# Performance work log

Hardware: AMD Instinct MI355X
Metric: run time of the kernel (lower is better)

## Reference

```python
import jax, jax.numpy as jnp
import numpy as np

DIM = 1024
HEADS = 16
DIM_HEAD = 64
INNER = HEADS * DIM_HEAD  # 1024
RANK = 16
ALPHA = 8.0
LORA_SCALE = ALPHA / RANK  # 0.5
NUM_PATCHES = 256
NUM_FRAMES = 8
T = NUM_PATCHES * NUM_FRAMES  # 2048
B = 2
MEM = 16
EPS = 1e-5


def _block_causal_mask(num_patches, num_frames):
    # generate_mask_matrix: causal across frames, full within a frame
    tril = np.tril(np.ones((num_frames, num_frames), dtype=np.int32))
    m = np.kron(tril, np.ones((num_patches, num_patches), dtype=np.int32))
    return jnp.asarray(m[None, None])  # [1,1,T,T]


def setup_inputs() -> dict:
    key = jax.random.key(0)
    ks = jax.random.split(key, 16)
    s_in = 1.0 / np.sqrt(DIM)
    s_r = 1.0 / np.sqrt(RANK)
    return {
        "x": jax.random.normal(ks[0], (B, T, DIM), jnp.float32),
        "memory_tokens": jax.random.normal(ks[1], (B, MEM, DIM), jnp.float32),
        "ln_g": jnp.ones((DIM,), jnp.float32),
        "ln_b": jnp.zeros((DIM,), jnp.float32),
        "w_qkv": jax.random.normal(ks[2], (DIM, 3 * INNER), jnp.float32) * s_in,
        "qA": jax.random.normal(ks[3], (DIM, RANK), jnp.float32) * s_in,
        "qB": jax.random.normal(ks[4], (RANK, INNER), jnp.float32) * s_r * 0.02,
        "kA": jax.random.normal(ks[5], (DIM, RANK), jnp.float32) * s_in,
        "kB": jax.random.normal(ks[6], (RANK, INNER), jnp.float32) * s_r * 0.02,
        "vA": jax.random.normal(ks[7], (DIM, RANK), jnp.float32) * s_in,
        "vB": jax.random.normal(ks[8], (RANK, INNER), jnp.float32) * s_r * 0.02,
        "w_out": jax.random.normal(ks[9], (INNER, DIM), jnp.float32) / np.sqrt(INNER),
        "b_out": jnp.zeros((DIM,), jnp.float32),
        "outA": jax.random.normal(ks[10], (INNER, RANK), jnp.float32) / np.sqrt(INNER),
        "outB": jax.random.normal(ks[11], (RANK, DIM), jnp.float32) * s_r * 0.02,
        "bias_mask": _block_causal_mask(NUM_PATCHES, NUM_FRAMES),
    }


def _lora(x, A, Bm):
    return LORA_SCALE * ((x @ A) @ Bm)


def reference(x, memory_tokens, ln_g, ln_b, w_qkv, qA, qB, kA, kB, vA, vB,
              w_out, b_out, outA, outB, bias_mask):
    # LayerNorm
    mu = jnp.mean(x, axis=-1, keepdims=True)
    var = jnp.var(x, axis=-1, keepdims=True)
    xn = (x - mu) * jax.lax.rsqrt(var + EPS) * ln_g + ln_b

    qkv = xn @ w_qkv  # [B,T,3*INNER]
    q, k, v = jnp.split(qkv, 3, axis=-1)
    # LoRA deltas (memory_tokens enables the LoRA path)
    q = q + _lora(xn, qA, qB)
    k = k + _lora(xn, kA, kB)
    v = v + _lora(xn, vA, vB)

    def to_heads(t):
        b, n, _ = t.shape
        return t.reshape(b, n, HEADS, DIM_HEAD).transpose(0, 2, 1, 3)  # b h n d

    q, k, v = to_heads(q), to_heads(k), to_heads(v)
    scale = DIM_HEAD ** -0.5
    dots = jnp.einsum('bhid,bhjd->bhij', q, k) * scale  # [B,H,T,T]
    dots = jnp.where(bias_mask[:, :, :q.shape[2], :q.shape[2]] == 0, -jnp.inf, dots)
    attn = jax.nn.softmax(dots, axis=-1)  # dropout p=0.0
    out = jnp.einsum('bhij,bhjd->bhid', attn, v)
    out = out.transpose(0, 2, 1, 3).reshape(x.shape[0], x.shape[1], INNER)
    out = out @ w_out + b_out
    out = out + _lora(out, outA, outB)  # lora_on_out
    return out
```

## Files before the change

### kernel.cpp

```cpp
#include <hip/hip_runtime.h>


#define DIMSZ 1024
#define TSEQ  2048
#define MTOK  4096

typedef __attribute__((ext_vector_type(8))) short bf16x8;
typedef __attribute__((ext_vector_type(4))) short bf16x4;
typedef __attribute__((ext_vector_type(4))) float f32x4;

__device__ __forceinline__ unsigned short f2bf(float f) {
  unsigned int u = __float_as_uint(f);
  u += 0x7fffu + ((u >> 16) & 1u);
  return (unsigned short)(u >> 16);
}
__device__ __forceinline__ float bf2f(unsigned short s) {
  return __uint_as_float(((unsigned int)s) << 16);
}
__device__ __forceinline__ unsigned int cvtpk_bf16(float a, float b) {
  unsigned int d;
  asm("v_cvt_pk_bf16_f32 %0, %1, %2" : "=v"(d) : "v"(a), "v"(b));
  return d;
}
__device__ __forceinline__ void gload16(const void* g, void* l) {
  __builtin_amdgcn_global_load_lds((const __attribute__((address_space(1))) void*)g,
                                   (__attribute__((address_space(3))) void*)l, 16, 0, 0);
}

__global__ __launch_bounds__(256) void ln_kernel(const float* __restrict__ x,
    const float* __restrict__ g, const float* __restrict__ b,
    unsigned short* __restrict__ xn) {
  int row = blockIdx.x;
  int tid = threadIdx.x;
  const float4* xr = (const float4*)(x + (size_t)row * DIMSZ);
  float4 v = xr[tid];
  float s  = v.x + v.y + v.z + v.w;
  float s2 = v.x*v.x + v.y*v.y + v.z*v.z + v.w*v.w;
  #pragma unroll
  for (int off = 32; off > 0; off >>= 1) {
    s  += __shfl_xor(s, off, 64);
    s2 += __shfl_xor(s2, off, 64);
  }
  __shared__ float red[8];
  int wid = tid >> 6, lane = tid & 63;
  if (lane == 0) { red[wid] = s; red[wid + 4] = s2; }
  __syncthreads();
  s  = red[0] + red[1] + red[2] + red[3];
  s2 = red[4] + red[5] + red[6] + red[7];
  float mu  = s * (1.0f / DIMSZ);
  float var = s2 * (1.0f / DIMSZ) - mu * mu;
  float rstd = rsqrtf(var + 1e-5f);
  float4 gg = ((const float4*)g)[tid];
  float4 bb = ((const float4*)b)[tid];
  ushort4 o;
  o.x = f2bf((v.x - mu) * rstd * gg.x + bb.x);
  o.y = f2bf((v.y - mu) * rstd * gg.y + bb.y);
  o.z = f2bf((v.z - mu) * rstd * gg.z + bb.z);
  o.w = f2bf((v.w - mu) * rstd * gg.w + bb.w);
  ((ushort4*)(xn + (size_t)row * DIMSZ))[tid] = o;
}

__global__ __launch_bounds__(64) void woutA_kernel(const float* __restrict__ w_out,
    const float* __restrict__ outA, float* __restrict__ WA) {
  int k = blockIdx.x;
  int l = threadIdx.x;
  float a[16];
  #pragma unroll
  for (int r = 0; r < 16; ++r) a[r] = 0.f;
  for (int c = l; c < DIMSZ; c += 64) {
    float w = w_out[(size_t)k * DIMSZ + c];
    const float* ap = outA + (size_t)c * 16;
    #pragma unroll
    for (int r = 0; r < 16; ++r) a[r] += w * ap[r];
  }
  #pragma unroll
  for (int r = 0; r < 16; ++r) {
    #pragma unroll
    for (int off = 32; off > 0; off >>= 1) a[r] += __shfl_xor(a[r], off, 64);
  }
  if (l < 16) WA[k * 16 + l] = a[l];
}

__global__ __launch_bounds__(256) void beff_kernel(const float* __restrict__ b_out,
    const float* __restrict__ outA, const float* __restrict__ outB,
    float* __restrict__ beff) {
  int tid = threadIdx.x, wid = tid >> 6, lane = tid & 63;
  float a[16];
  #pragma unroll
  for (int r = 0; r < 16; ++r) a[r] = 0.f;
  for (int c = tid; c < DIMSZ; c += 256) {
    float bo = b_out[c];
    const float* ap = outA + (size_t)c * 16;
    #pragma unroll
    for (int r = 0; r < 16; ++r) a[r] += bo * ap[r];
  }
  #pragma unroll
  for (int r = 0; r < 16; ++r) {
    #pragma unroll
    for (int off = 32; off > 0; off >>= 1) a[r] += __shfl_xor(a[r], off, 64);
  }
  __shared__ float sh[4][16];
  if (lane == 0) {
    #pragma unroll
    for (int r = 0; r < 16; ++r) sh[wid][r] = a[r];
  }
  __syncthreads();
  __shared__ float tt[16];
  if (tid < 16) tt[tid] = sh[0][tid] + sh[1][tid] + sh[2][tid] + sh[3][tid];
  __syncthreads();
  for (int n = tid; n < DIMSZ; n += 256) {
    float l = 0.f;
    #pragma unroll
    for (int r = 0; r < 16; ++r) l += tt[r] * outB[(size_t)r * DIMSZ + n];
    beff[n] = b_out[n] + 0.5f * l;
  }
}

__global__ __launch_bounds__(256) void foldT4_kernel(
    const float* __restrict__ w_qkv, const float* __restrict__ w_out,
    const float* __restrict__ qA, const float* __restrict__ qB,
    const float* __restrict__ kA, const float* __restrict__ kB,
    const float* __restrict__ vA, const float* __restrict__ vB,
    const float* __restrict__ WA, const float* __restrict__ outB,
    unsigned short* __restrict__ WqkvT, unsigned short* __restrict__ WoutT) {
  __shared__ float Bs[16][64];
  __shared__ unsigned short Ts[64][72];
  int z = blockIdx.z;
  const float *W, *A, *Bf;
  unsigned short* Wt;
  int ldw, col_off;
  if (z == 0)      { W = w_qkv; ldw = 3072; col_off = 0;    A = qA; Bf = qB;   Wt = WqkvT; }
  else if (z == 1) { W = w_qkv; ldw = 3072; col_off = 1024; A = kA; Bf = kB;   Wt = WqkvT + 1048576; }
  else if (z == 2) { W = w_qkv; ldw = 3072; col_off = 2048; A = vA; Bf = vB;   Wt = WqkvT + 2097152; }
  else             { W = w_out; ldw = 1024; col_off = 0;    A = WA; Bf = outB; Wt = WoutT; }
  int n0 = blockIdx.x * 64, k0 = blockIdx.y * 64;
  int tx = threadIdx.x, ty = threadIdx.y;
  for (int r = ty; r < 16; r += 4) Bs[r][tx] = Bf[(size_t)r * DIMSZ + n0 + tx];
  __syncthreads();
  for (int k = ty; k < 64; k += 4) {
    int kk = k0 + k;
    float w = W[(size_t)kk * ldw + col_off + n0 + tx];
    const float* Ar = A + (size_t)kk * 16;
    float lora = 0.f;
    #pragma unroll
    for (int r = 0; r < 16; ++r) lora += Ar[r] * Bs[r][tx];
    Ts[tx][k] = f2bf(w + 0.5f * lora);
  }
  __syncthreads();
  for (int n = ty; n < 64; n += 4)
    Wt[(size_t)(n0 + n) * DIMSZ + k0 + tx] = Ts[n][tx];
}

template<int MODE>
__global__ __launch_bounds__(256) void gemm_kernel(
    const unsigned short* __restrict__ Abf, const unsigned short* __restrict__ Bt,
    int K,
    unsigned short* __restrict__ Qo, unsigned short* __restrict__ Ko,
    unsigned short* __restrict__ Vto,
    const float* __restrict__ bias, float* __restrict__ Cout) {
  __shared__ __align__(16) char As[128 * 64 * 2];
  __shared__ __align__(16) char Bs[128 * 64 * 2];
  int n0 = blockIdx.x * 128;
  int m0 = blockIdx.y * 128;
  int tid = threadIdx.x;
  int wid = tid >> 6, lane = tid & 63;
  int wr = wid >> 1, wc = wid & 1;
  int hi = lane >> 4;
  f32x4 acc[4][4];
  #pragma unroll
  for (int i = 0; i < 4; ++i)
    #pragma unroll
    for (int j = 0; j < 4; ++j) acc[i][j] = (f32x4){0.f, 0.f, 0.f, 0.f};

  const char* gA = (const char*)Abf;
  const char* gB = (const char*)Bt;
  int Kb2 = K * 2;
  int nkt = K >> 6;
  for (int kt = 0; kt < nkt; ++kt) {
    #pragma unroll
    for (int j = 0; j < 4; ++j) {
      int it = wid * 4 + j;
      int p = it * 1024 + lane * 16;
      int row = p >> 7, colb = p & 127;
      int L = colb ^ ((row & 7) << 4);
      gload16(gA + (size_t)(m0 + row) * Kb2 + kt * 128 + L, As + it * 1024);
      gload16(gB + (size_t)(n0 + row) * Kb2 + kt * 128 + L, Bs + it * 1024);
    }
    __syncthreads();
    #pragma unroll
    for (int ks = 0; ks < 2; ++ks) {
      int kb = ks * 64 + hi * 16;
      bf16x8 af[4], bfr[4];
      #pragma unroll
      for (int m = 0; m < 4; ++m) {
        int row = wr * 64 + m * 16 + (lane & 15);
        af[m] = *(const bf16x8*)(As + row * 128 + (kb ^ ((row & 7) << 4)));
      }
      #pragma unroll
      for (int n = 0; n < 4; ++n) {
        int row = wc * 64 + n * 16 + (lane & 15);
        bfr[n] = *(const bf16x8*)(Bs + row * 128 + (kb ^ ((row & 7) << 4)));
      }
      __builtin_amdgcn_s_setprio(1);
      #pragma unroll
      for (int n = 0; n < 4; ++n)
        #pragma unroll
        for (int m = 0; m < 4; ++m)
          acc[n][m] = __builtin_amdgcn_mfma_f32_16x16x32_bf16(bfr[n], af[m], acc[n][m], 0, 0, 0);
      __builtin_amdgcn_s_setprio(0);
    }
    __syncthreads();
  }

  if (MODE == 0) {
    int sec  = n0 >> 10;
    int nloc = (n0 & 1023) + wc * 64;
    int h = nloc >> 6;
    int mbase = m0 + wr * 64;
    #pragma unroll
    for (int m = 0; m < 4; ++m) {
      int gm = mbase + m * 16 + (lane & 15);
      int bb = gm >> 11, t = gm & 2047;
      #pragma unroll
      for (int n = 0; n < 4; ++n) {
        int dloc = n * 16 + hi * 4;
        if (sec == 2) {
          #pragma unroll
          for (int r = 0; r < 4; ++r)
            Vto[((size_t)((bb * 16 + h) * 64 + dloc + r)) * TSEQ + t] = f2bf(acc[n][m][r]);
        } else {
          bf16x4 o;
          #pragma unroll
          for (int r = 0; r < 4; ++r) o[r] = (short)f2bf(acc[n][m][r]);
          size_t idx = ((size_t)(bb * 16 + h) * TSEQ + t) * 64 + dloc;
          *(bf16x4*)((sec == 0 ? Qo : Ko) + idx) = o;
        }
      }
    }
  } else {
    int mbase = m0 + wr * 64;
    int nbase = n0 + wc * 64;
    #pragma unroll
    for (int m = 0; m < 4; ++m) {
      int t = mbase + m * 16 + (lane & 15);
      #pragma unroll
      for (int n = 0; n < 4; ++n) {
        int c = nbase + n * 16 + hi * 4;
        float4 bs = *(const float4*)(bias + c);
        float4 o;
        o.x = acc[n][m][0] + bs.x;
        o.y = acc[n][m][1] + bs.y;
        o.z = acc[n][m][2] + bs.z;
        o.w = acc[n][m][3] + bs.w;
        *(float4*)(Cout + (size_t)t * DIMSZ + c) = o;
      }
    }
  }
}

__global__ __launch_bounds__(256, 4) void attn_kernel(
    const unsigned short* __restrict__ Qg, const unsigned short* __restrict__ Kg,
    const unsigned short* __restrict__ Vt, unsigned short* __restrict__ Orow) {
  __shared__ __align__(16) char KsB[2][64 * 128];
  __shared__ __align__(16) char VsB[2][64 * 128];
  __shared__ __align__(16) char Ps[4][16 * 128];
  int bh = blockIdx.x;
  int y  = blockIdx.y;
  int qt = (y < 16) ? (31 - y) : (y - 16);
  int b = bh >> 4, h = bh & 15;
  int tid = threadIdx.x, wid = tid >> 6, lane = tid & 63;
  int hi = lane >> 4, lo = lane & 15;
  const char* Qb = (const char*)(Qg + (size_t)bh * TSEQ * 64);
  const char* Kb = (const char*)(Kg + (size_t)bh * TSEQ * 64);
  const char* Vb = (const char*)(Vt + (size_t)bh * 64 * TSEQ);
  int q0 = qt * 64;

  int srow = tid >> 3;
  int scol = ((tid & 7) << 4) ^ ((srow & 7) << 4);

  const float qscale = 0.18033688f;
  bf16x8 qf[2];
  {
    int row = q0 + wid * 16 + lo;
    #pragma unroll
    for (int ks = 0; ks < 2; ++ks) {
      bf16x8 raw = *(const bf16x8*)(Qb + (size_t)row * 128 + ks * 64 + hi * 16);
      bf16x8 sc;
      #pragma unroll
      for (int i = 0; i < 8; ++i)
        sc[i] = (short)f2bf(bf2f((unsigned short)raw[i]) * qscale);
      qf[ks] = sc;
    }
  }

  f32x4 Oacc[4];
  #pragma unroll
  for (int df = 0; df < 4; ++df) Oacc[df] = (f32x4){0.f, 0.f, 0.f, 0.f};
  float mrun = -INFINITY, lrun = 0.f;

  char* Pw = Ps[wid];
  char* pbase = Pw + lo * 128;
  int pswz = (lo & 7) << 4;

  int nkt = ((qt >> 2) + 1) << 2;

  {
    const char* ksrc = Kb + (size_t)srow * 128 + scol;
    gload16(ksrc,               KsB[0] + tid * 16);
    gload16(ksrc + 32 * 128,    KsB[0] + tid * 16 + 4096);
    const char* vsrc = Vb + (size_t)srow * (TSEQ * 2) + scol;
    gload16(vsrc,               VsB[0] + tid * 16);
    gload16(vsrc + 32 * (TSEQ * 2), VsB[0] + tid * 16 + 4096);
  }

  for (int kt = 0; kt < nkt; ++kt) {
    __syncthreads();
    if (kt + 1 < nkt) {
      int k0n = (kt + 1) << 6;
      char* kd = KsB[(kt + 1) & 1];
      const char* ksrc = Kb + (size_t)(k0n + srow) * 128 + scol;
      gload16(ksrc,            kd + tid * 16);
      gload16(ksrc + 32 * 128, kd + tid * 16 + 4096);
    }
    if (kt) {
      char* vd = VsB[kt & 1];
      const char* vsrc = Vb + (size_t)srow * (TSEQ * 2) + (kt << 7) + scol;
      gload16(vsrc,                   vd + tid * 16);
      gload16(vsrc + 32 * (TSEQ * 2), vd + tid * 16 + 4096);
    }
    const char* Kbuf = KsB[kt & 1];

    f32x4 s[4];
    #pragma unroll
    for (int nf = 0; nf < 4; ++nf) s[nf] = (f32x4){0.f, 0.f, 0.f, 0.f};
    #pragma unroll
    for (int ks = 0; ks < 2; ++ks) {
      int kb = ks * 64 + hi * 16;
      bf16x8 kf[4];
      #pragma unroll
      for (int nf = 0; nf < 4; ++nf) {
        int row = nf * 16 + lo;
        kf[nf] = *(const bf16x8*)(Kbuf + row * 128 + (kb ^ ((row & 7) << 4)));
      }
      __builtin_amdgcn_s_setprio(1);
      #pragma unroll
      for (int nf = 0; nf < 4; ++nf)
        s[nf] = __builtin_amdgcn_mfma_f32_16x16x32_bf16(kf[nf], qf[ks], s[nf], 0, 0, 0);
      __builtin_amdgcn_s_setprio(0);
    }

    if (kt) {
      const char* Vbuf = VsB[(kt - 1) & 1];
      #pragma unroll
      for (int ks2 = 0; ks2 < 2; ++ks2) {
        int kb = ks2 * 64 + hi * 16;
        bf16x8 pf = *(const bf16x8*)(Pw + lo * 128 + (kb ^ pswz));
        bf16x8 vf[4];
        #pragma unroll
        for (int df = 0; df < 4; ++df) {
          int row = df * 16 + lo;
          vf[df] = *(const bf16x8*)(Vbuf + row * 128 + (kb ^ ((row & 7) << 4)));
        }
        __builtin_amdgcn_s_setprio(1);
        #pragma unroll
        for (int df = 0; df < 4; ++df)
          Oacc[df] = __builtin_amdgcn_mfma_f32_16x16x32_bf16(vf[df], pf, Oacc[df], 0, 0, 0);
        __builtin_amdgcn_s_setprio(0);
      }
    }

    float a0 = fmaxf(fmaxf(s[0][0], s[0][1]), fmaxf(s[0][2], s[0][3]));
    float a1 = fmaxf(fmaxf(s[1][0], s[1][1]), fmaxf(s[1][2], s[1][3]));
    float a2 = fmaxf(fmaxf(s[2][0], s[2][1]), fmaxf(s[2][2], s[2][3]));
    float a3 = fmaxf(fmaxf(s[3][0], s[3][1]), fmaxf(s[3][2], s[3][3]));
    float mx = fmaxf(fmaxf(a0, a1), fmaxf(a2, a3));
    mx = fmaxf(mx, __shfl_xor(mx, 16, 64));
    mx = fmaxf(mx, __shfl_xor(mx, 32, 64));

    if (!__all(mx <= mrun + 8.0f)) {
      float mn = fmaxf(mrun, mx);
      float al = exp2f(mrun - mn);
      mrun = mn;
      lrun *= al;
      #pragma unroll
      for (int df = 0; df < 4; ++df)
        #pragma unroll
        for (int r = 0; r < 4; ++r) Oacc[df][r] *= al;
    }

    float rs0 = 0.f, rs1 = 0.f, rs2 = 0.f, rs3 = 0.f;
    #pragma unroll
    for (int nf = 0; nf < 4; ++nf) {
      float p0 = exp2f(s[nf][0] - mrun);
      float p1 = exp2f(s[nf][1] - mrun);
      float p2 = exp2f(s[nf][2] - mrun);
      float p3 = exp2f(s[nf][3] - mrun);
      s[nf][0] = p0; s[nf][1] = p1; s[nf][2] = p2; s[nf][3] = p3;
      rs0 += p0; rs1 += p1; rs2 += p2; rs3 += p3;
    }
    lrun += (rs0 + rs1) + (rs2 + rs3);

    #pragma unroll
    for (int nf = 0; nf < 4; ++nf) {
      unsigned int w0 = cvtpk_bf16(s[nf][0], s[nf][1]);
      unsigned int w1 = cvtpk_bf16(s[nf][2], s[nf][3]);
      uint2 pr; pr.x = w0; pr.y = w1;
      *(uint2*)(pbase + ((nf * 32 + hi * 8) ^ pswz)) = pr;
    }
  }

  __syncthreads();
  {
    const char* Vbuf = VsB[(nkt - 1) & 1];
    #pragma unroll
    for (int ks2 = 0; ks2 < 2; ++ks2) {
      int kb = ks2 * 64 + hi * 16;
      bf16x8 pf = *(const bf16x8*)(Pw + lo * 128 + (kb ^ pswz));
      bf16x8 vf[4];
      #pragma unroll
      for (int df = 0; df < 4; ++df) {
        int row = df * 16 + lo;
        vf[df] = *(const bf16x8*)(Vbuf + row * 128 + (kb ^ ((row & 7) << 4)));
      }
      __builtin_amdgcn_s_setprio(1);
      #pragma unroll
      for (int df = 0; df < 4; ++df)
        Oacc[df] = __builtin_amdgcn_mfma_f32_16x16x32_bf16(vf[df], pf, Oacc[df], 0, 0, 0);
      __builtin_amdgcn_s_setprio(0);
    }
  }

  lrun += __shfl_xor(lrun, 16, 64);
  lrun += __shfl_xor(lrun, 32, 64);
  float inv = 1.0f / lrun;
  int t = q0 + wid * 16 + lo;
  size_t rowbase = ((size_t)(b * TSEQ + t)) * DIMSZ + h * 64;
  #pragma unroll
  for (int df = 0; df < 4; ++df) {
    bf16x4 o;
    #pragma unroll
    for (int r = 0; r < 4; ++r) o[r] = (short)f2bf(Oacc[df][r] * inv);
    *(bf16x4*)(Orow + rowbase + df * 16 + hi * 4) = o;
  }
}

extern "C" void kernel_launch(void* const* d_in, const int* in_sizes, int n_in,
                              void* d_out, int out_size, void* d_ws, size_t ws_size,
                              hipStream_t stream) {
  (void)in_sizes; (void)n_in; (void)out_size; (void)ws_size;
  const float* x     = (const float*)d_in[0];
  const float* ln_g  = (const float*)d_in[2];
  const float* ln_b  = (const float*)d_in[3];
  const float* w_qkv = (const float*)d_in[4];
  const float* qA    = (const float*)d_in[5];
  const float* qB    = (const float*)d_in[6];
  const float* kA    = (const float*)d_in[7];
  const float* kB    = (const float*)d_in[8];
  const float* vA    = (const float*)d_in[9];
  const float* vB    = (const float*)d_in[10];
  const float* w_out = (const float*)d_in[11];
  const float* b_out = (const float*)d_in[12];
  const float* outA  = (const float*)d_in[13];
  const float* outB  = (const float*)d_in[14];

  char* ws = (char*)d_ws;
  unsigned short* xn    = (unsigned short*)(ws);
  unsigned short* WqkvT = (unsigned short*)(ws + 8388608);
  unsigned short* WoutT = (unsigned short*)(ws + 14680064);
  float*          WA    = (float*)(ws + 16777216);
  float*          beff  = (float*)(ws + 16842752);
  unsigned short* Qb    = (unsigned short*)(ws + 16846848);
  unsigned short* Kb    = (unsigned short*)(ws + 25235456);
  unsigned short* Vtb   = (unsigned short*)(ws + 33624064);
  unsigned short* Orow  = xn;
  float* outp = (float*)d_out;

  ln_kernel<<<MTOK, 256, 0, stream>>>(x, ln_g, ln_b, xn);
  woutA_kernel<<<DIMSZ, 64, 0, stream>>>(w_out, outA, WA);
  beff_kernel<<<1, 256, 0, stream>>>(b_out, outA, outB, beff);
  dim3 fb(64, 4);
  foldT4_kernel<<<dim3(16, 16, 4), fb, 0, stream>>>(w_qkv, w_out, qA, qB, kA, kB,
                                                    vA, vB, WA, outB, WqkvT, WoutT);

  gemm_kernel<0><<<dim3(24, 32), 256, 0, stream>>>(xn, WqkvT, DIMSZ, Qb, Kb, Vtb, nullptr, nullptr);
  attn_kernel<<<dim3(32, 32), 256, 0, stream>>>(Qb, Kb, Vtb, Orow);
  gemm_kernel<1><<<dim3(8, 32), 256, 0, stream>>>(Orow, WoutT, DIMSZ, nullptr, nullptr, nullptr, beff, outp);
}
```

Measured before the change: 142.9 us.

## Double attention query tile per wave and merge prep kernels into one launch

The attention kernel now gives each wave 32 query rows (two 16-row MFMA fragments) instead of 16. Each K/V tile loaded into LDS is therefore reused across twice as many queries, and the grid is halved. Separately, layernorm, the w_out·outA fold and the effective-bias computation are merged into one launch to cut launch overhead. In exchange, register pressure roughly doubles (launch bounds drop to 2 blocks per SM). Coarser 128-row tiles also waste more work on the block-causal boundary and leave fewer blocks to balance the load.

```diff
diff --git a/kernel.cpp b/kernel.cpp
--- a/kernel.cpp
+++ b/kernel.cpp
@@ -27,92 +27,88 @@
                                    (__attribute__((address_space(3))) void*)l, 16, 0, 0);
 }
 
-__global__ __launch_bounds__(256) void ln_kernel(const float* __restrict__ x,
-    const float* __restrict__ g, const float* __restrict__ b,
-    unsigned short* __restrict__ xn) {
-  int row = blockIdx.x;
-  int tid = threadIdx.x;
-  const float4* xr = (const float4*)(x + (size_t)row * DIMSZ);
-  float4 v = xr[tid];
-  float s  = v.x + v.y + v.z + v.w;
-  float s2 = v.x*v.x + v.y*v.y + v.z*v.z + v.w*v.w;
-  #pragma unroll
-  for (int off = 32; off > 0; off >>= 1) {
-    s  += __shfl_xor(s, off, 64);
-    s2 += __shfl_xor(s2, off, 64);
-  }
+__global__ __launch_bounds__(256) void prep_kernel(const float* __restrict__ x,
+    const float* __restrict__ g, const float* __restrict__ bln,
+    const float* __restrict__ w_out, const float* __restrict__ outA,
+    const float* __restrict__ b_out, const float* __restrict__ outB,
+    unsigned short* __restrict__ xn, float* __restrict__ WA,
+    float* __restrict__ beff) {
   __shared__ float red[8];
-  int wid = tid >> 6, lane = tid & 63;
-  if (lane == 0) { red[wid] = s; red[wid + 4] = s2; }
-  __syncthreads();
-  s  = red[0] + red[1] + red[2] + red[3];
-  s2 = red[4] + red[5] + red[6] + red[7];
-  float mu  = s * (1.0f / DIMSZ);
-  float var = s2 * (1.0f / DIMSZ) - mu * mu;
-  float rstd = rsqrtf(var + 1e-5f);
-  float4 gg = ((const float4*)g)[tid];
-  float4 bb = ((const float4*)b)[tid];
-  ushort4 o;
-  o.x = f2bf((v.x - mu) * rstd * gg.x + bb.x);
-  o.y = f2bf((v.y - mu) * rstd * gg.y + bb.y);
-  o.z = f2bf((v.z - mu) * rstd * gg.z + bb.z);
-  o.w = f2bf((v.w - mu) * rstd * gg.w + bb.w);
-  ((ushort4*)(xn + (size_t)row * DIMSZ))[tid] = o;
-}
-
-__global__ __launch_bounds__(64) void woutA_kernel(const float* __restrict__ w_out,
-    const float* __restrict__ outA, float* __restrict__ WA) {
-  int k = blockIdx.x;
-  int l = threadIdx.x;
-  float a[16];
-  #pragma unroll
-  for (int r = 0; r < 16; ++r) a[r] = 0.f;
-  for (int c = l; c < DIMSZ; c += 64) {
-    float w = w_out[(size_t)k * DIMSZ + c];
-    const float* ap = outA + (size_t)c * 16;
-    #pragma unroll
-    for (int r = 0; r < 16; ++r) a[r] += w * ap[r];
-  }
-  #pragma unroll
-  for (int r = 0; r < 16; ++r) {
-    #pragma unroll
-    for (int off = 32; off > 0; off >>= 1) a[r] += __shfl_xor(a[r], off, 64);
-  }
-  if (l < 16) WA[k * 16 + l] = a[l];
-}
-
-__global__ __launch_bounds__(256) void beff_kernel(const float* __restrict__ b_out,
-    const float* __restrict__ outA, const float* __restrict__ outB,
-    float* __restrict__ beff) {
+  __shared__ float sh[4][16];
+  __shared__ float tt[16];
+  int bid = blockIdx.x;
   int tid = threadIdx.x, wid = tid >> 6, lane = tid & 63;
-  float a[16];
-  #pragma unroll
-  for (int r = 0; r < 16; ++r) a[r] = 0.f;
-  for (int c = tid; c < DIMSZ; c += 256) {
-    float bo = b_out[c];
-    const float* ap = outA + (size_t)c * 16;
-    #pragma unroll
-    for (int r = 0; r < 16; ++r) a[r] += bo * ap[r];
-  }
-  #pragma unroll
-  for (int r = 0; r < 16; ++r) {
-    #pragma unroll
-    for (int off = 32; off > 0; off >>= 1) a[r] += __shfl_xor(a[r], off, 64);
-  }
-  __shared__ float sh[4][16];
-  if (lane == 0) {
-    #pragma unroll
-    for (int r = 0; r < 16; ++r) sh[wid][r] = a[r];
-  }
-  __syncthreads();
-  __shared__ float tt[16];
-  if (tid < 16) tt[tid] = sh[0][tid] + sh[1][tid] + sh[2][tid] + sh[3][tid];
-  __syncthreads();
-  for (int n = tid; n < DIMSZ; n += 256) {
-    float l = 0.f;
-    #pragma unroll
-    for (int r = 0; r < 16; ++r) l += tt[r] * outB[(size_t)r * DIMSZ + n];
-    beff[n] = b_out[n] + 0.5f * l;
+  if (bid < MTOK) {
+    int row = bid;
+    const float4* xr = (const float4*)(x + (size_t)row * DIMSZ);
+    float4 v = xr[tid];
+    float s  = v.x + v.y + v.z + v.w;
+    float s2 = v.x*v.x + v.y*v.y + v.z*v.z + v.w*v.w;
+    #pragma unroll
+    for (int off = 32; off > 0; off >>= 1) {
+      s  += __shfl_xor(s, off, 64);
+      s2 += __shfl_xor(s2, off, 64);
+    }
+    if (lane == 0) { red[wid] = s; red[wid + 4] = s2; }
+    __syncthreads();
+    s  = red[0] + red[1] + red[2] + red[3];
+    s2 = red[4] + red[5] + red[6] + red[7];
+    float mu  = s * (1.0f / DIMSZ);
+    float var = s2 * (1.0f / DIMSZ) - mu * mu;
+    float rstd = rsqrtf(var + 1e-5f);
+    float4 gg = ((const float4*)g)[tid];
+    float4 bb = ((const float4*)bln)[tid];
+    ushort4 o;
+    o.x = f2bf((v.x - mu) * rstd * gg.x + bb.x);
+    o.y = f2bf((v.y - mu) * rstd * gg.y + bb.y);
+    o.z = f2bf((v.z - mu) * rstd * gg.z + bb.z);
+    o.w = f2bf((v.w - mu) * rstd * gg.w + bb.w);
+    ((ushort4*)(xn + (size_t)row * DIMSZ))[tid] = o;
+  } else if (bid < MTOK + 256) {
+    int k = (bid - MTOK) * 4 + wid;
+    float a[16];
+    #pragma unroll
+    for (int r = 0; r < 16; ++r) a[r] = 0.f;
+    for (int c = lane; c < DIMSZ; c += 64) {
+      float w = w_out[(size_t)k * DIMSZ + c];
+      const float* ap = outA + (size_t)c * 16;
+      #pragma unroll
+      for (int r = 0; r < 16; ++r) a[r] += w * ap[r];
+    }
+    #pragma unroll
+    for (int r = 0; r < 16; ++r) {
+      #pragma unroll
+      for (int off = 32; off > 0; off >>= 1) a[r] += __shfl_xor(a[r], off, 64);
+    }
+    if (lane < 16) WA[k * 16 + lane] = a[lane];
+  } else {
+    float a[16];
+    #pragma unroll
+    for (int r = 0; r < 16; ++r) a[r] = 0.f;
+    for (int c = tid; c < DIMSZ; c += 256) {
+      float bo = b_out[c];
+      const float* ap = outA + (size_t)c * 16;
+      #pragma unroll
+      for (int r = 0; r < 16; ++r) a[r] += bo * ap[r];
+    }
+    #pragma unroll
+    for (int r = 0; r < 16; ++r) {
+      #pragma unroll
+      for (int off = 32; off > 0; off >>= 1) a[r] += __shfl_xor(a[r], off, 64);
+    }
+    if (lane == 0) {
+      #pragma unroll
+      for (int r = 0; r < 16; ++r) sh[wid][r] = a[r];
+    }
+    __syncthreads();
+    if (tid < 16) tt[tid] = sh[0][tid] + sh[1][tid] + sh[2][tid] + sh[3][tid];
+    __syncthreads();
+    for (int n = tid; n < DIMSZ; n += 256) {
+      float l = 0.f;
+      #pragma unroll
+      for (int r = 0; r < 16; ++r) l += tt[r] * outB[(size_t)r * DIMSZ + n];
+      beff[n] = b_out[n] + 0.5f * l;
+    }
   }
 }
 
@@ -258,30 +254,31 @@
   }
 }
 
-__global__ __launch_bounds__(256, 4) void attn_kernel(
+__global__ __launch_bounds__(256, 2) void attn_kernel(
     const unsigned short* __restrict__ Qg, const unsigned short* __restrict__ Kg,
     const unsigned short* __restrict__ Vt, unsigned short* __restrict__ Orow) {
   __shared__ __align__(16) char KsB[2][64 * 128];
   __shared__ __align__(16) char VsB[2][64 * 128];
-  __shared__ __align__(16) char Ps[4][16 * 128];
+  __shared__ __align__(16) char Ps[4][32 * 128];
   int bh = blockIdx.x;
   int y  = blockIdx.y;
-  int qt = (y < 16) ? (31 - y) : (y - 16);
+  int qt = (y < 8) ? (15 - y) : (y - 8);
   int b = bh >> 4, h = bh & 15;
   int tid = threadIdx.x, wid = tid >> 6, lane = tid & 63;
   int hi = lane >> 4, lo = lane & 15;
   const char* Qb = (const char*)(Qg + (size_t)bh * TSEQ * 64);
   const char* Kb = (const char*)(Kg + (size_t)bh * TSEQ * 64);
   const char* Vb = (const char*)(Vt + (size_t)bh * 64 * TSEQ);
-  int q0 = qt * 64;
+  int q0 = qt * 128;
 
   int srow = tid >> 3;
   int scol = ((tid & 7) << 4) ^ ((srow & 7) << 4);
 
   const float qscale = 0.18033688f;
-  bf16x8 qf[2];
-  {
-    int row = q0 + wid * 16 + lo;
+  bf16x8 qf[2][2];
+  #pragma unroll
+  for (int m = 0; m < 2; ++m) {
+    int row = q0 + wid * 32 + m * 16 + lo;
     #pragma unroll
     for (int ks = 0; ks < 2; ++ks) {
       bf16x8 raw = *(const bf16x8*)(Qb + (size_t)row * 128 + ks * 64 + hi * 16);
@@ -289,20 +286,22 @@
       #pragma unroll
       for (int i = 0; i < 8; ++i)
         sc[i] = (short)f2bf(bf2f((unsigned short)raw[i]) * qscale);
-      qf[ks] = sc;
-    }
-  }
-
-  f32x4 Oacc[4];
+      qf[m][ks] = sc;
+    }
+  }
+
+  f32x4 Oacc[2][4];
   #pragma unroll
-  for (int df = 0; df < 4; ++df) Oacc[df] = (f32x4){0.f, 0.f, 0.f, 0.f};
-  float mrun = -INFINITY, lrun = 0.f;
+  for (int m = 0; m < 2; ++m)
+    #pragma unroll
+    for (int df = 0; df < 4; ++df) Oacc[m][df] = (f32x4){0.f, 0.f, 0.f, 0.f};
+  float mrun[2] = {-INFINITY, -INFINITY};
+  float lrun[2] = {0.f, 0.f};
 
   char* Pw = Ps[wid];
-  char* pbase = Pw + lo * 128;
   int pswz = (lo & 7) << 4;
 
-  int nkt = ((qt >> 2) + 1) << 2;
+  int nkt = ((qt >> 1) + 1) << 2;
 
   {
     const char* ksrc = Kb + (size_t)srow * 128 + scol;
@@ -330,9 +329,11 @@
     }
     const char* Kbuf = KsB[kt & 1];
 
-    f32x4 s[4];
-    #pragma unroll
-    for (int nf = 0; nf < 4; ++nf) s[nf] = (f32x4){0.f, 0.f, 0.f, 0.f};
+    f32x4 s[2][4];
+    #pragma unroll
+    for (int m = 0; m < 2; ++m)
+      #pragma unroll
+      for (int nf = 0; nf < 4; ++nf) s[m][nf] = (f32x4){0.f, 0.f, 0.f, 0.f};
     #pragma unroll
     for (int ks = 0; ks < 2; ++ks) {
       int kb = ks * 64 + hi * 16;
@@ -344,8 +345,10 @@
       }
       __builtin_amdgcn_s_setprio(1);
       #pragma unroll
-      for (int nf = 0; nf < 4; ++nf)
-        s[nf] = __builtin_amdgcn_mfma_f32_16x16x32_bf16(kf[nf], qf[ks], s[nf], 0, 0, 0);
+      for (int m = 0; m < 2; ++m)
+        #pragma unroll
+        for (int nf = 0; nf < 4; ++nf)
+          s[m][nf] = __builtin_amdgcn_mfma_f32_16x16x32_bf16(kf[nf], qf[m][ks], s[m][nf], 0, 0, 0);
       __builtin_amdgcn_s_setprio(0);
     }
 
@@ -354,8 +357,10 @@
       #pragma unroll
       for (int ks2 = 0; ks2 < 2; ++ks2) {
         int kb = ks2 * 64 + hi * 16;
-        bf16x8 pf = *(const bf16x8*)(Pw + lo * 128 + (kb ^ pswz));
-        bf16x8 vf[4];
+        bf16x8 pf[2], vf[4];
+        #pragma unroll
+        for (int m = 0; m < 2; ++m)
+          pf[m] = *(const bf16x8*)(Pw + (m * 16 + lo) * 128 + (kb ^ pswz));
         #pragma unroll
         for (int df = 0; df < 4; ++df) {
           int row = df * 16 + lo;
@@ -363,49 +368,61 @@
         }
         __builtin_amdgcn_s_setprio(1);
         #pragma unroll
+        for (int m = 0; m < 2; ++m)
+          #pragma unroll
+          for (int df = 0; df < 4; ++df)
+            Oacc[m][df] = __builtin_amdgcn_mfma_f32_16x16x32_bf16(vf[df], pf[m], Oacc[m][df], 0, 0, 0);
+        __builtin_amdgcn_s_setprio(0);
+      }
+    }
+
+    float mx[2];
+    #pragma unroll
+    for (int m = 0; m < 2; ++m) {
+      float a0 = fmaxf(fmaxf(s[m][0][0], s[m][0][1]), fmaxf(s[m][0][2], s[m][0][3]));
+      float a1 = fmaxf(fmaxf(s[m][1][0], s[m][1][1]), fmaxf(s[m][1][2], s[m][1][3]));
+      float a2 = fmaxf(fmaxf(s[m][2][0], s[m][2][1]), fmaxf(s[m][2][2], s[m][2][3]));
+      float a3 = fmaxf(fmaxf(s[m][3][0], s[m][3][1]), fmaxf(s[m][3][2], s[m][3][3]));
+      float v = fmaxf(fmaxf(a0, a1), fmaxf(a2, a3));
+      v = fmaxf(v, __shfl_xor(v, 16, 64));
+      v = fmaxf(v, __shfl_xor(v, 32, 64));
+      mx[m] = v;
+    }
+    int ok = (mx[0] <= mrun[0] + 8.0f) & (mx[1] <= mrun[1] + 8.0f);
+    if (!__all(ok)) {
+      #pragma unroll
+      for (int m = 0; m < 2; ++m) {
+        float mn = fmaxf(mrun[m], mx[m]);
+        float al = exp2f(mrun[m] - mn);
+        mrun[m] = mn;
+        lrun[m] *= al;
+        #pragma unroll
         for (int df = 0; df < 4; ++df)
-          Oacc[df] = __builtin_amdgcn_mfma_f32_16x16x32_bf16(vf[df], pf, Oacc[df], 0, 0, 0);
-        __builtin_amdgcn_s_setprio(0);
-      }
-    }
-
-    float a0 = fmaxf(fmaxf(s[0][0], s[0][1]), fmaxf(s[0][2], s[0][3]));
-    float a1 = fmaxf(fmaxf(s[1][0], s[1][1]), fmaxf(s[1][2], s[1][3]));
-    float a2 = fmaxf(fmaxf(s[2][0], s[2][1]), fmaxf(s[2][2], s[2][3]));
-    float a3 = fmaxf(fmaxf(s[3][0], s[3][1]), fmaxf(s[3][2], s[3][3]));
-    float mx = fmaxf(fmaxf(a0, a1), fmaxf(a2, a3));
-    mx = fmaxf(mx, __shfl_xor(mx, 16, 64));
-    mx = fmaxf(mx, __shfl_xor(mx, 32, 64));
-
-    if (!__all(mx <= mrun + 8.0f)) {
-      float mn = fmaxf(mrun, mx);
-      float al = exp2f(mrun - mn);
-      mrun = mn;
-      lrun *= al;
-      #pragma unroll
-      for (int df = 0; df < 4; ++df)
-        #pragma unroll
-        for (int r = 0; r < 4; ++r) Oacc[df][r] *= al;
-    }
-
-    float rs0 = 0.f, rs1 = 0.f, rs2 = 0.f, rs3 = 0.f;
-    #pragma unroll
-    for (int nf = 0; nf < 4; ++nf) {
-      float p0 = exp2f(s[nf][0] - mrun);
-      float p1 = exp2f(s[nf][1] - mrun);
-      float p2 = exp2f(s[nf][2] - mrun);
-      float p3 = exp2f(s[nf][3] - mrun);
-      s[nf][0] = p0; s[nf][1] = p1; s[nf][2] = p2; s[nf][3] = p3;
-      rs0 += p0; rs1 += p1; rs2 += p2; rs3 += p3;
-    }
-    lrun += (rs0 + rs1) + (rs2 + rs3);
-
-    #pragma unroll
-    for (int nf = 0; nf < 4; ++nf) {
-      unsigned int w0 = cvtpk_bf16(s[nf][0], s[nf][1]);
-      unsigned int w1 = cvtpk_bf16(s[nf][2], s[nf][3]);
-      uint2 pr; pr.x = w0; pr.y = w1;
-      *(uint2*)(pbase + ((nf * 32 + hi * 8) ^ pswz)) = pr;
+          #pragma unroll
+          for (int r = 0; r < 4; ++r) Oacc[m][df][r] *= al;
+      }
+    }
+    #pragma unroll
+    for (int m = 0; m < 2; ++m) {
+      float rs0 = 0.f, rs1 = 0.f, rs2 = 0.f, rs3 = 0.f;
+      #pragma unroll
+      for (int nf = 0; nf < 4; ++nf) {
+        float p0 = exp2f(s[m][nf][0] - mrun[m]);
+        float p1 = exp2f(s[m][nf][1] - mrun[m]);
+        float p2 = exp2f(s[m][nf][2] - mrun[m]);
+        float p3 = exp2f(s[m][nf][3] - mrun[m]);
+        s[m][nf][0] = p0; s[m][nf][1] = p1; s[m][nf][2] = p2; s[m][nf][3] = p3;
+        rs0 += p0; rs1 += p1; rs2 += p2; rs3 += p3;
+      }
+      lrun[m] += (rs0 + rs1) + (rs2 + rs3);
+      char* pbase = Pw + (m * 16 + lo) * 128;
+      #pragma unroll
+      for (int nf = 0; nf < 4; ++nf) {
+        uint2 pr;
+        pr.x = cvtpk_bf16(s[m][nf][0], s[m][nf][1]);
+        pr.y = cvtpk_bf16(s[m][nf][2], s[m][nf][3]);
+        *(uint2*)(pbase + ((nf * 32 + hi * 8) ^ pswz)) = pr;
+      }
     }
   }
 
@@ -415,8 +432,10 @@
     #pragma unroll
     for (int ks2 = 0; ks2 < 2; ++ks2) {
       int kb = ks2 * 64 + hi * 16;
-      bf16x8 pf = *(const bf16x8*)(Pw + lo * 128 + (kb ^ pswz));
-      bf16x8 vf[4];
+      bf16x8 pf[2], vf[4];
+      #pragma unroll
+      for (int m = 0; m < 2; ++m)
+        pf[m] = *(const bf16x8*)(Pw + (m * 16 + lo) * 128 + (kb ^ pswz));
       #pragma unroll
       for (int df = 0; df < 4; ++df) {
         int row = df * 16 + lo;
@@ -424,23 +443,29 @@
       }
       __builtin_amdgcn_s_setprio(1);
       #pragma unroll
-      for (int df = 0; df < 4; ++df)
-        Oacc[df] = __builtin_amdgcn_mfma_f32_16x16x32_bf16(vf[df], pf, Oacc[df], 0, 0, 0);
+      for (int m = 0; m < 2; ++m)
+        #pragma unroll
+        for (int df = 0; df < 4; ++df)
+          Oacc[m][df] = __builtin_amdgcn_mfma_f32_16x16x32_bf16(vf[df], pf[m], Oacc[m][df], 0, 0, 0);
       __builtin_amdgcn_s_setprio(0);
     }
   }
 
-  lrun += __shfl_xor(lrun, 16, 64);
-  lrun += __shfl_xor(lrun, 32, 64);
-  float inv = 1.0f / lrun;
-  int t = q0 + wid * 16 + lo;
-  size_t rowbase = ((size_t)(b * TSEQ + t)) * DIMSZ + h * 64;
   #pragma unroll
-  for (int df = 0; df < 4; ++df) {
-    bf16x4 o;
-    #pragma unroll
-    for (int r = 0; r < 4; ++r) o[r] = (short)f2bf(Oacc[df][r] * inv);
-    *(bf16x4*)(Orow + rowbase + df * 16 + hi * 4) = o;
+  for (int m = 0; m < 2; ++m) {
+    float l = lrun[m];
+    l += __shfl_xor(l, 16, 64);
+    l += __shfl_xor(l, 32, 64);
+    float inv = 1.0f / l;
+    int t = q0 + wid * 32 + m * 16 + lo;
+    size_t rowbase = ((size_t)(b * TSEQ + t)) * DIMSZ + h * 64;
+    #pragma unroll
+    for (int df = 0; df < 4; ++df) {
+      bf16x4 o;
+      #pragma unroll
+      for (int r = 0; r < 4; ++r) o[r] = (short)f2bf(Oacc[m][df][r] * inv);
+      *(bf16x4*)(Orow + rowbase + df * 16 + hi * 4) = o;
+    }
   }
 }
 
@@ -475,14 +500,13 @@
   unsigned short* Orow  = xn;
   float* outp = (float*)d_out;
 
-  ln_kernel<<<MTOK, 256, 0, stream>>>(x, ln_g, ln_b, xn);
-  woutA_kernel<<<DIMSZ, 64, 0, stream>>>(w_out, outA, WA);
-  beff_kernel<<<1, 256, 0, stream>>>(b_out, outA, outB, beff);
+  prep_kernel<<<MTOK + 257, 256, 0, stream>>>(x, ln_g, ln_b, w_out, outA, b_out,
+                                              outB, xn, WA, beff);
   dim3 fb(64, 4);
   foldT4_kernel<<<dim3(16, 16, 4), fb, 0, stream>>>(w_qkv, w_out, qA, qB, kA, kB,
                                                     vA, vB, WA, outB, WqkvT, WoutT);
 
   gemm_kernel<0><<<dim3(24, 32), 256, 0, stream>>>(xn, WqkvT, DIMSZ, Qb, Kb, Vtb, nullptr, nullptr);
-  attn_kernel<<<dim3(32, 32), 256, 0, stream>>>(Qb, Kb, Vtb, Orow);
+  attn_kernel<<<dim3(32, 16), 256, 0, stream>>>(Qb, Kb, Vtb, Orow);
   gemm_kernel<1><<<dim3(8, 32), 256, 0, stream>>>(Orow, WoutT, DIMSZ, nullptr, nullptr, nullptr, beff, outp);
 }
```

Measured after the change: 154.7 us. 1.08x slower.
